# Kernel optimization log

Measured on AMD Instinct MI355X. Metric: run time of the kernel, lower is better.

## Reference

```python
import jax, jax.numpy as jnp
import numpy as np
from jax import lax


def setup_inputs() -> dict:
    key = jax.random.key(0)
    k1, k2 = jax.random.split(key)
    x = jax.random.normal(k1, (32, 256, 64, 64), dtype=jnp.float32)
    conv_w = jax.random.normal(k2, (1, 1, 3), dtype=jnp.float32) * 0.5  # Conv1d(1,1,3,bias=False) weight [out=1,in=1,k=3]
    return {"x": x, "conv_w": conv_w}


def reference(x, conv_w):
    # x: [b, c, h, w]
    # Global average pool -> [b, c]
    y = jnp.mean(x, axis=(2, 3))
    # Conv1d over the channel axis (PyTorch cross-correlation), SAME padding
    y = lax.conv_general_dilated(
        y[:, None, :],          # [b, 1, c]
        conv_w,                 # [1, 1, 3]
        window_strides=(1,),
        padding="SAME",
        dimension_numbers=("NCH", "OIH", "NCH"),
    )[:, 0, :]                  # [b, c]
    att = jax.nn.sigmoid(y)
    # Top-3 channels per sample (largest, sorted), then batched gather
    _, idx = lax.top_k(att, 3)                              # [b, 3]
    out = jnp.take_along_axis(x, idx[:, :, None, None], axis=1)  # [b, 3, h, w]
    return out
```

## Files before the change

kernel.cpp:

```cpp
#include <hip/hip_runtime.h>

#define B  32
#define C  256
#define HW 4096
#define BC (B * C)

__global__ __launch_bounds__(256) void eca_mean_kernel(
    const float* __restrict__ x, float* __restrict__ means) {
    const int wid  = (blockIdx.x * 256 + threadIdx.x) >> 6;
    const int lane = threadIdx.x & 63;
    const float4* x4 = reinterpret_cast<const float4*>(x);

#pragma unroll
    for (int s = 0; s < 2; ++s) {
        const int slice = wid * 2 + s;
        const float4* p4 = x4 + (size_t)slice * (HW / 4);
        float s0 = 0.f, s1 = 0.f, s2 = 0.f, s3 = 0.f;
#pragma unroll
        for (int i = 0; i < 4; ++i) {
            float4 a = p4[lane + (4 * i + 0) * 64];
            float4 b = p4[lane + (4 * i + 1) * 64];
            float4 c = p4[lane + (4 * i + 2) * 64];
            float4 d = p4[lane + (4 * i + 3) * 64];
            s0 += (a.x + a.y) + (a.z + a.w);
            s1 += (b.x + b.y) + (b.z + b.w);
            s2 += (c.x + c.y) + (c.z + c.w);
            s3 += (d.x + d.y) + (d.z + d.w);
        }
        float sum = (s0 + s1) + (s2 + s3);
#pragma unroll
        for (int off = 32; off > 0; off >>= 1)
            sum += __shfl_xor(sum, off);
        if (lane == 0) means[slice] = sum * (1.0f / HW);
    }
}

__global__ __launch_bounds__(256) void eca_fused_kernel(
    const float* __restrict__ x, const float* __restrict__ means,
    const float* __restrict__ w, float* __restrict__ out) {
    const int b  = blockIdx.x / 12;
    const int j  = blockIdx.x % 12;
    const int jj = j >> 2;
    const int q  = j & 3;
    const int c  = threadIdx.x;
    const int wave = c >> 6;

    const float* m = means + b * C;
    const float ym1 = (c > 0)     ? m[c - 1] : 0.f;
    const float y0  = m[c];
    const float yp1 = (c < C - 1) ? m[c + 1] : 0.f;
    const float y = w[0] * ym1 + w[1] * y0 + w[2] * yp1;

    unsigned int u = __float_as_uint(y);
    u = (u & 0x80000000u) ? ~u : (u | 0x80000000u);
    const unsigned long long key =
        ((unsigned long long)u << 8) | (unsigned long long)(255 - c);

    __shared__ unsigned long long cand[12];

    bool excluded = false;
#pragma unroll
    for (int r = 0; r < 3; ++r) {
        unsigned long long k = excluded ? 0ULL : key;
#pragma unroll
        for (int off = 32; off > 0; off >>= 1) {
            unsigned long long o = __shfl_xor(k, off);
            k = (o > k) ? o : k;
        }
        if ((c & 63) == 0) cand[wave * 3 + r] = k;
        if (key == k) excluded = true;
    }
    __syncthreads();

    unsigned long long k0 = 0, k1 = 0, k2 = 0;
#pragma unroll
    for (int i = 0; i < 12; ++i) {
        const unsigned long long v = cand[i];
        if (v > k0)      { k2 = k1; k1 = k0; k0 = v; }
        else if (v > k1) { k2 = k1; k1 = v; }
        else if (v > k2) { k2 = v; }
    }
    const unsigned long long kw = (jj == 0) ? k0 : (jj == 1) ? k1 : k2;
    const int mych = 255 - (int)(kw & 0xFFULL);

    const float4* src = reinterpret_cast<const float4*>(
        x + ((size_t)(b * C + mych)) * HW);
    float4* dst = reinterpret_cast<float4*>(
        out + ((size_t)(b * 3 + jj)) * HW);
    const int o = q * 256 + c;
    dst[o] = src[o];
}

extern "C" void kernel_launch(void* const* d_in, const int* in_sizes, int n_in,
                              void* d_out, int out_size, void* d_ws, size_t ws_size,
                              hipStream_t stream) {
    const float* x      = (const float*)d_in[0];
    const float* conv_w = (const float*)d_in[1];
    float* out = (float*)d_out;

    float* means = (float*)d_ws;

    eca_mean_kernel<<<BC / 8, 256, 0, stream>>>(x, means);
    eca_fused_kernel<<<B * 12, 256, 0, stream>>>(x, means, conv_w, out);
}
```

Baseline: 29.28 us.

## Fuse mean, top-k and gather into one kernel with per-batch completion flags

```diff
diff --git a/kernel.cpp b/kernel.cpp
--- a/kernel.cpp
+++ b/kernel.cpp
@@ -1,29 +1,36 @@
 #include <hip/hip_runtime.h>
 
-#define B  32
-#define C  256
-#define HW 4096
-#define BC (B * C)
+#define B    32
+#define C    256
+#define HW   4096
+#define BC   (B * C)
+#define NBLK 1024
 
-__global__ __launch_bounds__(256) void eca_mean_kernel(
-    const float* __restrict__ x, float* __restrict__ means) {
-    const int wid  = (blockIdx.x * 256 + threadIdx.x) >> 6;
-    const int lane = threadIdx.x & 63;
+__global__ __launch_bounds__(256, 4) void eca_one_kernel(
+    const float* __restrict__ x, const float* __restrict__ w,
+    float* means, unsigned int* ctr, unsigned int* flag,
+    float* __restrict__ out) {
+    const int g    = blockIdx.x;
+    const int tid  = threadIdx.x;
+    const int lane = tid & 63;
+    const int wave = tid >> 6;
+    const int b    = g >> 5;
+
     const float4* x4 = reinterpret_cast<const float4*>(x);
 
 #pragma unroll
     for (int s = 0; s < 2; ++s) {
-        const int slice = wid * 2 + s;
+        const int slice = g * 8 + wave * 2 + s;
         const float4* p4 = x4 + (size_t)slice * (HW / 4);
         float s0 = 0.f, s1 = 0.f, s2 = 0.f, s3 = 0.f;
 #pragma unroll
         for (int i = 0; i < 4; ++i) {
             float4 a = p4[lane + (4 * i + 0) * 64];
-            float4 b = p4[lane + (4 * i + 1) * 64];
+            float4 bb = p4[lane + (4 * i + 1) * 64];
             float4 c = p4[lane + (4 * i + 2) * 64];
             float4 d = p4[lane + (4 * i + 3) * 64];
             s0 += (a.x + a.y) + (a.z + a.w);
-            s1 += (b.x + b.y) + (b.z + b.w);
+            s1 += (bb.x + bb.y) + (bb.z + bb.w);
             s2 += (c.x + c.y) + (c.z + c.w);
             s3 += (d.x + d.y) + (d.z + d.w);
         }
@@ -31,64 +38,83 @@
 #pragma unroll
         for (int off = 32; off > 0; off >>= 1)
             sum += __shfl_xor(sum, off);
-        if (lane == 0) means[slice] = sum * (1.0f / HW);
-    }
-}
-
-__global__ __launch_bounds__(256) void eca_fused_kernel(
-    const float* __restrict__ x, const float* __restrict__ means,
-    const float* __restrict__ w, float* __restrict__ out) {
-    const int b  = blockIdx.x / 12;
-    const int j  = blockIdx.x % 12;
-    const int jj = j >> 2;
-    const int q  = j & 3;
-    const int c  = threadIdx.x;
-    const int wave = c >> 6;
-
-    const float* m = means + b * C;
-    const float ym1 = (c > 0)     ? m[c - 1] : 0.f;
-    const float y0  = m[c];
-    const float yp1 = (c < C - 1) ? m[c + 1] : 0.f;
-    const float y = w[0] * ym1 + w[1] * y0 + w[2] * yp1;
-
-    unsigned int u = __float_as_uint(y);
-    u = (u & 0x80000000u) ? ~u : (u | 0x80000000u);
-    const unsigned long long key =
-        ((unsigned long long)u << 8) | (unsigned long long)(255 - c);
-
-    __shared__ unsigned long long cand[12];
-
-    bool excluded = false;
-#pragma unroll
-    for (int r = 0; r < 3; ++r) {
-        unsigned long long k = excluded ? 0ULL : key;
-#pragma unroll
-        for (int off = 32; off > 0; off >>= 1) {
-            unsigned long long o = __shfl_xor(k, off);
-            k = (o > k) ? o : k;
-        }
-        if ((c & 63) == 0) cand[wave * 3 + r] = k;
-        if (key == k) excluded = true;
+        if (lane == 0) atomicExch(&means[slice], sum * (1.0f / HW));
     }
     __syncthreads();
 
-    unsigned long long k0 = 0, k1 = 0, k2 = 0;
+    __shared__ unsigned int sdone;
+    if (tid == 0) {
+        __threadfence();
+        sdone = (atomicAdd(&ctr[b], 1u) == NBLK / B - 1) ? 1u : 0u;
+    }
+    __syncthreads();
+    const bool finisher = (sdone != 0u);
+
+    __shared__ float m_lds[C];
+    __shared__ unsigned long long cand[12];
+    if (finisher) {
+        m_lds[tid] = atomicAdd(&means[b * C + tid], 0.0f);
+        __syncthreads();
+        const float ym1 = (tid > 0)     ? m_lds[tid - 1] : 0.f;
+        const float y0  = m_lds[tid];
+        const float yp1 = (tid < C - 1) ? m_lds[tid + 1] : 0.f;
+        const float y = w[0] * ym1 + w[1] * y0 + w[2] * yp1;
+
+        unsigned int u = __float_as_uint(y);
+        u = (u & 0x80000000u) ? ~u : (u | 0x80000000u);
+        const unsigned long long key =
+            ((unsigned long long)u << 8) | (unsigned long long)(255 - tid);
+
+        bool excluded = false;
 #pragma unroll
-    for (int i = 0; i < 12; ++i) {
-        const unsigned long long v = cand[i];
-        if (v > k0)      { k2 = k1; k1 = k0; k0 = v; }
-        else if (v > k1) { k2 = k1; k1 = v; }
-        else if (v > k2) { k2 = v; }
+        for (int r = 0; r < 3; ++r) {
+            unsigned long long k = excluded ? 0ULL : key;
+#pragma unroll
+            for (int off = 32; off > 0; off >>= 1) {
+                unsigned long long o = __shfl_xor(k, off);
+                k = (o > k) ? o : k;
+            }
+            if ((tid & 63) == 0) cand[wave * 3 + r] = k;
+            if (key == k) excluded = true;
+        }
+        __syncthreads();
+
+        if (tid == 0) {
+            unsigned long long k0 = 0, k1 = 0, k2 = 0;
+#pragma unroll
+            for (int i = 0; i < 12; ++i) {
+                const unsigned long long v = cand[i];
+                if (v > k0)      { k2 = k1; k1 = k0; k0 = v; }
+                else if (v > k1) { k2 = k1; k1 = v; }
+                else if (v > k2) { k2 = v; }
+            }
+            const unsigned int i0 = 255u - (unsigned int)(k0 & 0xFFULL);
+            const unsigned int i1 = 255u - (unsigned int)(k1 & 0xFFULL);
+            const unsigned int i2 = 255u - (unsigned int)(k2 & 0xFFULL);
+            const unsigned int packed =
+                0x80000000u | (i0 << 16) | (i1 << 8) | i2;
+            atomicExch(&flag[b], packed);
+        }
     }
-    const unsigned long long kw = (jj == 0) ? k0 : (jj == 1) ? k1 : k2;
-    const int mych = 255 - (int)(kw & 0xFFULL);
 
-    const float4* src = reinterpret_cast<const float4*>(
-        x + ((size_t)(b * C + mych)) * HW);
-    float4* dst = reinterpret_cast<float4*>(
-        out + ((size_t)(b * 3 + jj)) * HW);
-    const int o = q * 256 + c;
-    dst[o] = src[o];
+    __shared__ unsigned int spacked;
+    if (tid == 0) {
+        unsigned int p;
+        while ((((p = atomicOr(&flag[b], 0u))) & 0x80000000u) == 0u)
+            __builtin_amdgcn_s_sleep(8);
+        spacked = p;
+    }
+    __syncthreads();
+    const unsigned int packed = spacked;
+
+    if (tid < 96) {
+        const int g4 = g * 96 + tid;
+        const int bj = g4 >> 10;
+        const int jj = bj - (bj / 3) * 3;
+        const int ch = (int)((packed >> (16 - 8 * jj)) & 0xFFu);
+        float4* out4 = reinterpret_cast<float4*>(out);
+        out4[g4] = x4[(size_t)(b * C + ch) * (HW / 4) + (g4 & (HW / 4 - 1))];
+    }
 }
 
 extern "C" void kernel_launch(void* const* d_in, const int* in_sizes, int n_in,
@@ -98,8 +124,11 @@
     const float* conv_w = (const float*)d_in[1];
     float* out = (float*)d_out;
 
-    float* means = (float*)d_ws;
+    float*        means = (float*)d_ws;
+    unsigned int* ctr   = (unsigned int*)((char*)d_ws + BC * sizeof(float));
+    unsigned int* flag  = ctr + 32;
 
-    eca_mean_kernel<<<BC / 8, 256, 0, stream>>>(x, means);
-    eca_fused_kernel<<<B * 12, 256, 0, stream>>>(x, means, conv_w, out);
+    hipMemsetAsync((void*)ctr, 0, 64 * sizeof(unsigned int), stream);
+
+    eca_one_kernel<<<NBLK, 256, 0, stream>>>(x, conv_w, means, ctr, flag, out);
 }
```

New measurement: 66.17 us. +126.0%, slower.
